# Performance work log

Hardware: AMD Instinct MI355X
Metric: run time of the kernel (lower is better)

The kernel has to match this reference:

```python
import jax, jax.numpy as jnp
from jax import lax
import numpy as np


def _sobel(x):
    """|sobel_x(x)| + |sobel_y(x)| with zero padding. x: [N,C,H,W].
    Implemented as ONE depthwise conv (replaces the per-batch/per-channel
    conv2d loops in the torch Sobelxy module; math is identical)."""
    N, C, H, W = x.shape
    kx = jnp.array([[-1., 0., 1.], [-2., 0., 2.], [-1., 0., 1.]], x.dtype)
    ky = jnp.array([[1., 2., 1.], [0., 0., 0.], [-1., -2., -1.]], x.dtype)
    k = jnp.tile(jnp.stack([kx, ky]), (C, 1, 1))[:, None]  # [2C,1,3,3]
    o = lax.conv_general_dilated(x, k, (1, 1), ((1, 1), (1, 1)),
                                 feature_group_count=C)  # [N,2C,H,W]
    o = o.reshape(N, C, 2, H, W)
    return jnp.abs(o[:, :, 0]) + jnp.abs(o[:, :, 1])


def setup_inputs() -> dict:
    B, C, H, W, NL = 4, 1, 640, 640, 10
    key = jax.random.key(0)
    k1, k2, k3, k4 = jax.random.split(key, 4)
    image_vis = jax.random.uniform(k1, (B, C, H, W), jnp.float32)
    image_ir = jax.random.uniform(k2, (B, 1, H, W), jnp.float32)
    generate_img = jax.random.uniform(k3, (B, C, H, W), jnp.float32)
    LW_th = jax.random.uniform(k4, (B, 1, H, W), jnp.float32)
    # labels: (cls, x1, y1, x2, y2); all-zero coords => ignored box
    rng = np.random.default_rng(0)
    lab = np.zeros((B, NL, 5), np.int32)
    for bi in range(B):
        n = int(rng.integers(3, NL + 1))
        x1 = rng.integers(0, W // 2, n)
        y1 = rng.integers(0, H // 2, n)
        x2 = np.minimum(x1 + rng.integers(16, W // 2, n), W)
        y2 = np.minimum(y1 + rng.integers(16, H // 2, n), H)
        lab[bi, :n, 1] = x1; lab[bi, :n, 2] = y1
        lab[bi, :n, 3] = x2; lab[bi, :n, 4] = y2
    return {"b": jnp.float32(0.5), "c": jnp.float32(0.5),
            "image_vis": image_vis, "image_ir": image_ir,
            "generate_img": generate_img, "label": jnp.asarray(lab),
            "LW_th": LW_th}


def reference(b, c, image_vis, image_ir, generate_img, label, LW_th):
    alpha, beta = b, c
    B, C, H, W = image_vis.shape
    NL = label.shape[1]
    image_y = image_vis
    image_th = jnp.broadcast_to(LW_th, (B, C, H, W))

    x_in_mean = 0.5 * image_y + 0.5 * image_th
    x_in_mean_7 = 0.3 * image_y + 0.7 * image_th
    x_in_mean_max = jnp.maximum(image_y, x_in_mean)

    y_grad = _sobel(image_y)
    x_in_mean_grad = _sobel(x_in_mean)
    gen_grad = _sobel(generate_img)
    x_grad_joint = jnp.maximum(y_grad, x_in_mean_grad)

    # global per-sample L1 losses (F.l1_loss per batch element = mean over CHW)
    loss_in = jnp.mean(jnp.abs(generate_img - x_in_mean_max), axis=(1, 2, 3))
    loss_grad = jnp.mean(jnp.abs(gen_grad - x_grad_joint), axis=(1, 2, 3))
    loss_global = alpha * loss_in + (1 - alpha) * loss_grad

    # ---- per-box losses via masking (exactly equals crop + zero-padded Sobel:
    # Sobel(crop) inside the box == Sobel(mask*image) inside the box) ----
    x1 = label[..., 1]; y1 = label[..., 2]  # [B,NL]
    x2 = label[..., 3]; y2 = label[..., 4]
    valid = ~((x1 == 0) & (y1 == 0) & (x2 == 0) & (y2 == 0))
    rows = jnp.arange(H); cols = jnp.arange(W)
    rmask = (rows[None, None, :] >= y1[..., None]) & (rows[None, None, :] < y2[..., None])
    cmask = (cols[None, None, :] >= x1[..., None]) & (cols[None, None, :] < x2[..., None])
    mask = (rmask[..., :, None] & cmask[..., None, :]).astype(image_y.dtype)  # [B,NL,H,W]
    mask5 = mask[:, :, None]  # [B,NL,1,H,W]

    def boxed(img):  # [B,C,H,W] -> masked [B*NL,C,H,W]
        return (img[:, None] * mask5).reshape(B * NL, C, H, W)

    m_vis = boxed(image_y)
    m_mean = boxed(x_in_mean_7)
    m_gen = boxed(generate_img)
    g_vis = _sobel(m_vis)
    g_mean = _sobel(m_mean)
    g_gen = _sobel(m_gen)
    g_max = jnp.maximum(g_vis, g_mean)
    in_max = jnp.maximum(m_vis, m_mean)

    fmask = mask.reshape(B * NL, 1, H, W)
    area = ((y2 - y1) * (x2 - x1)).reshape(B * NL).astype(image_y.dtype) * C
    safe_area = jnp.maximum(area, 1.0)
    Lssim = jnp.sum(jnp.abs(g_gen - g_max) * fmask, axis=(1, 2, 3)) / safe_area
    L1loss = jnp.sum(jnp.abs(m_gen - in_max) * fmask, axis=(1, 2, 3)) / safe_area
    v = valid.reshape(B * NL).astype(image_y.dtype)
    Lssim = (Lssim * v).reshape(B, NL)
    L1loss = (L1loss * v).reshape(B, NL)

    exist = ((Lssim != 0) | (L1loss != 0)).astype(image_y.dtype)
    cnt = exist.sum(axis=1)
    safe_cnt = jnp.maximum(cnt, 1.0)
    ls = jnp.where(cnt > 0, Lssim.sum(axis=1) / safe_cnt, 0.0)
    lin = jnp.where(cnt > 0, L1loss.sum(axis=1) / safe_cnt, 0.0)
    loss_label = (1 - beta) * ls + beta * lin

    loss_ss = jnp.zeros((B,), image_y.dtype)
    return (loss_ss, loss_global, loss_label, loss_in, loss_grad, ls, lin)
```

## Files before the change

### kernel.cpp

```cpp
#include <hip/hip_runtime.h>

#define BB    4
#define HH    640
#define WW    640
#define NLB   10
#define HWSZ  (HH * WW)
#define BLK   128
#define PR    8
#define GT    5
#define GBANDS (HH / PR)
#define GPB   (GT * GBANDS)
#define GBLK  (GPB * BB)
#define BOXSLOTS 40
#define XBLK  (BB * NLB * BOXSLOTS)

__device__ __forceinline__ void reduce2_write(float vin, float vgr,
                                              float* __restrict__ dst) {
    #pragma unroll
    for (int off = 32; off > 0; off >>= 1) {
        vin += __shfl_down(vin, off);
        vgr += __shfl_down(vgr, off);
    }
    __shared__ float s0[2], s1[2];
    const int lane = threadIdx.x & 63;
    const int w    = threadIdx.x >> 6;
    if (lane == 0) { s0[w] = vin; s1[w] = vgr; }
    __syncthreads();
    if (threadIdx.x == 0) {
        dst[0] = s0[0] + s0[1];
        dst[1] = s1[0] + s1[1];
    }
}

#define SOB(P, S) \
    (fabsf((P[S][2] - P[S][0]) + 2.0f * (P[S+1][2] - P[S+1][0]) + (P[S+2][2] - P[S+2][0])) + \
     fabsf((P[S][0] + 2.0f * P[S][1] + P[S][2]) - (P[S+2][0] + 2.0f * P[S+2][1] + P[S+2][2])))

__global__ __launch_bounds__(BLK) void kmain(const float* __restrict__ vis,
                                             const float* __restrict__ th,
                                             const float* __restrict__ gen,
                                             const int* __restrict__ label,
                                             float* __restrict__ gpart,
                                             float* __restrict__ xpart) {
    const int t = threadIdx.x;
    if (blockIdx.x < GBLK) {
        const int gid  = blockIdx.x;
        const int b    = gid / GPB;
        const int rem  = gid % GPB;
        const int band = rem / GT;
        const int xt   = rem % GT;
        const int c    = xt * BLK + t;
        const int r0   = band * PR;
        const float* v = vis + b * HWSZ;
        const float* tp = th + b * HWSZ;
        const float* g = gen + b * HWSZ;
        const bool okL = (c >= 1);
        const bool okR = (c + 1 < WW);

        float rv[PR + 2][3], rt[PR + 2][3], rg[PR + 2][3];
        #pragma unroll
        for (int i = 0; i < PR + 2; ++i) {
            const int rr = r0 - 1 + i;
            const bool rok = ((unsigned)rr < (unsigned)HH);
            const int base = rr * WW + c;
            rv[i][0] = (rok && okL) ? v[base - 1]  : 0.0f;
            rv[i][1] =  rok         ? v[base]      : 0.0f;
            rv[i][2] = (rok && okR) ? v[base + 1]  : 0.0f;
            rt[i][0] = (rok && okL) ? tp[base - 1] : 0.0f;
            rt[i][1] =  rok         ? tp[base]     : 0.0f;
            rt[i][2] = (rok && okR) ? tp[base + 1] : 0.0f;
            rg[i][0] = (rok && okL) ? g[base - 1]  : 0.0f;
            rg[i][1] =  rok         ? g[base]      : 0.0f;
            rg[i][2] = (rok && okR) ? g[base + 1]  : 0.0f;
        }
        float t_in = 0.0f, t_gr = 0.0f;
        #pragma unroll
        for (int s = 0; s < PR; ++s) {
            float m[3][3];
            #pragma unroll
            for (int i = 0; i < 3; ++i)
                #pragma unroll
                for (int j = 0; j < 3; ++j)
                    m[i][j] = 0.5f * rv[s + i][j] + 0.5f * rt[s + i][j];
            const float sv = SOB(rv, s);
            const float sg = SOB(rg, s);
            const float sm = SOB(m, 0);
            t_gr += fabsf(sg - fmaxf(sv, sm));
            t_in += fabsf(rg[s + 1][1] - fmaxf(rv[s + 1][1], m[1][1]));
        }
        reduce2_write(t_in, t_gr, gpart + gid * 2);
    } else {
        const int q    = blockIdx.x - GBLK;
        const int box  = q / BOXSLOTS;
        const int slot = q % BOXSLOTS;
        const int b    = box / NLB;
        const int* lb  = label + box * 5;
        const int x1 = lb[1], y1 = lb[2], x2 = lb[3], y2 = lb[4];
        const float* v = vis + b * HWSZ;
        const float* tp = th + b * HWSZ;
        const float* g = gen + b * HWSZ;
        float t_in = 0.0f, t_gr = 0.0f;
        for (int r0 = y1 + slot * PR; r0 < y2; r0 += BOXSLOTS * PR) {
            for (int cb = x1; cb < x2; cb += BLK) {
                const int c = cb + t;
                const bool okL = (c > x1) && (c - 1 < x2);
                const bool okC = (c < x2);
                const bool okR = (c + 1 < x2);
                float rv[PR + 2][3], rt[PR + 2][3], rg[PR + 2][3];
                #pragma unroll
                for (int i = 0; i < PR + 2; ++i) {
                    const int rr = r0 - 1 + i;
                    const bool rok = (rr >= y1) && (rr < y2);
                    const int base = rr * WW + c;
                    rv[i][0] = (rok && okL) ? v[base - 1]  : 0.0f;
                    rv[i][1] = (rok && okC) ? v[base]      : 0.0f;
                    rv[i][2] = (rok && okR) ? v[base + 1]  : 0.0f;
                    rt[i][0] = (rok && okL) ? tp[base - 1] : 0.0f;
                    rt[i][1] = (rok && okC) ? tp[base]     : 0.0f;
                    rt[i][2] = (rok && okR) ? tp[base + 1] : 0.0f;
                    rg[i][0] = (rok && okL) ? g[base - 1]  : 0.0f;
                    rg[i][1] = (rok && okC) ? g[base]      : 0.0f;
                    rg[i][2] = (rok && okR) ? g[base + 1]  : 0.0f;
                }
                #pragma unroll
                for (int s = 0; s < PR; ++s) {
                    const float inb = (okC && (r0 + s < y2)) ? 1.0f : 0.0f;
                    float m[3][3];
                    #pragma unroll
                    for (int i = 0; i < 3; ++i)
                        #pragma unroll
                        for (int j = 0; j < 3; ++j)
                            m[i][j] = 0.3f * rv[s + i][j] + 0.7f * rt[s + i][j];
                    const float sv = SOB(rv, s);
                    const float sg = SOB(rg, s);
                    const float sm = SOB(m, 0);
                    t_gr += inb * fabsf(sg - fmaxf(sv, sm));
                    t_in += inb * fabsf(rg[s + 1][1] - fmaxf(rv[s + 1][1], m[1][1]));
                }
            }
        }
        reduce2_write(t_in, t_gr, xpart + q * 2);
    }
}

__global__ __launch_bounds__(256) void kfin(const float* __restrict__ gpart,
                                            const float* __restrict__ xpart,
                                            const int* __restrict__ label,
                                            const float* __restrict__ bptr,
                                            const float* __restrict__ cptr,
                                            float* __restrict__ out) {
    const int t = threadIdx.x;
    __shared__ float Sin[BB], Sgr[BB];
    __shared__ float Ls[BB * NLB], L1[BB * NLB];
    {
        const int w = t >> 6, l = t & 63;
        float a = 0.0f, gr = 0.0f;
        for (int j = l; j < GPB; j += 64) {
            a  += gpart[(w * GPB + j) * 2 + 0];
            gr += gpart[(w * GPB + j) * 2 + 1];
        }
        #pragma unroll
        for (int off = 32; off > 0; off >>= 1) {
            a  += __shfl_down(a, off);
            gr += __shfl_down(gr, off);
        }
        if (l == 0) { Sin[w] = a; Sgr[w] = gr; }
    }
    if (t < BB * NLB) {
        float si = 0.0f, sg = 0.0f;
        for (int s = 0; s < BOXSLOTS; ++s) {
            si += xpart[(t * BOXSLOTS + s) * 2 + 0];
            sg += xpart[(t * BOXSLOTS + s) * 2 + 1];
        }
        const int* lb = label + t * 5;
        const int x1 = lb[1], y1 = lb[2], x2 = lb[3], y2 = lb[4];
        const bool valid = !((x1 == 0) && (y1 == 0) && (x2 == 0) && (y2 == 0));
        const float area = (float)((y2 - y1) * (x2 - x1));
        const float safe_area = fmaxf(area, 1.0f);
        const float vv = valid ? 1.0f : 0.0f;
        Ls[t] = sg / safe_area * vv;
        L1[t] = si / safe_area * vv;
    }
    __syncthreads();
    if (t < BB) {
        const float alpha = bptr[0];
        const float beta  = cptr[0];
        float cnt = 0.0f, sls = 0.0f, slin = 0.0f;
        for (int nl = 0; nl < NLB; nl++) {
            const float a = Ls[t * NLB + nl];
            const float l = L1[t * NLB + nl];
            if (a != 0.0f || l != 0.0f) cnt += 1.0f;
            sls  += a;
            slin += l;
        }
        const float safe_cnt = fmaxf(cnt, 1.0f);
        const float ls  = (cnt > 0.0f) ? (sls  / safe_cnt) : 0.0f;
        const float lin = (cnt > 0.0f) ? (slin / safe_cnt) : 0.0f;
        const float loss_label = (1.0f - beta) * ls + beta * lin;
        const float loss_in    = Sin[t] * (1.0f / (float)HWSZ);
        const float loss_grad  = Sgr[t] * (1.0f / (float)HWSZ);
        const float loss_global = alpha * loss_in + (1.0f - alpha) * loss_grad;
        out[0      + t] = 0.0f;
        out[BB     + t] = loss_global;
        out[2 * BB + t] = loss_label;
        out[3 * BB + t] = loss_in;
        out[4 * BB + t] = loss_grad;
        out[5 * BB + t] = ls;
        out[6 * BB + t] = lin;
    }
}

extern "C" void kernel_launch(void* const* d_in, const int* in_sizes, int n_in,
                              void* d_out, int out_size, void* d_ws, size_t ws_size,
                              hipStream_t stream) {
    const float* bptr  = (const float*)d_in[0];
    const float* cptr  = (const float*)d_in[1];
    const float* vis   = (const float*)d_in[2];
    const float* gen   = (const float*)d_in[4];
    const int*   label = (const int*)d_in[5];
    const float* th    = (const float*)d_in[6];
    float* out = (float*)d_out;

    float* gpart = (float*)d_ws;
    float* xpart = gpart + GBLK * 2;

    kmain<<<GBLK + XBLK, BLK, 0, stream>>>(vis, th, gen, label, gpart, xpart);
    kfin<<<1, 256, 0, stream>>>(gpart, xpart, label, bptr, cptr, out);
}
```

Measured before the change: 117.5 us.

## Compute 4x4 pixel strips per thread with float4 loads and linear Sobel of the blend

Each thread now covers a 4-column by 4-row strip instead of one column by 8 rows. It loads each input row with one aligned float4 plus two scalar edge values, which cuts the redundant overlapping neighbour loads of the old one-column layout. The blended image's Sobel gradients are built as weighted sums of the vis and th gradients, so the blended 3x3 window is no longer formed separately. The global-sum path launches half as many blocks, and the box path aligns its start column to 4. In exchange each thread holds more registers, and many threads in box blocks sit idle because a block now spans 512 columns.

```diff
diff --git a/kernel.cpp b/kernel.cpp
--- a/kernel.cpp
+++ b/kernel.cpp
@@ -1,18 +1,19 @@
 #include <hip/hip_runtime.h>
 
-#define BB    4
-#define HH    640
-#define WW    640
-#define NLB   10
-#define HWSZ  (HH * WW)
-#define BLK   128
-#define PR    8
-#define GT    5
-#define GBANDS (HH / PR)
-#define GPB   (GT * GBANDS)
-#define GBLK  (GPB * BB)
-#define BOXSLOTS 40
-#define XBLK  (BB * NLB * BOXSLOTS)
+#define BB     4
+#define HH     640
+#define WW     640
+#define NLB    10
+#define HWSZ   (HH * WW)
+#define BLK    128
+#define PRX    4
+#define GXT    160
+#define GBANDS 160
+#define GSIDS  (BB * GBANDS * GXT)
+#define GBLKS  (GSIDS / BLK)
+#define GPBB   (GBLKS / BB)
+#define SLOTS  40
+#define XBLKS  (BB * NLB * SLOTS)
 
 __device__ __forceinline__ void reduce2_write(float vin, float vgr,
                                               float* __restrict__ dst) {
@@ -32,9 +33,71 @@
     }
 }
 
-#define SOB(P, S) \
-    (fabsf((P[S][2] - P[S][0]) + 2.0f * (P[S+1][2] - P[S+1][0]) + (P[S+2][2] - P[S+2][0])) + \
-     fabsf((P[S][0] + 2.0f * P[S][1] + P[S][2]) - (P[S+2][0] + 2.0f * P[S+2][1] + P[S+2][2])))
+__device__ __forceinline__ void strip4(const float* __restrict__ v,
+                                       const float* __restrict__ t,
+                                       const float* __restrict__ g,
+                                       int c0, int r0, int ry1, int ry2,
+                                       int cx1, int cx2, float w0, float w1,
+                                       float& s_in, float& s_gr) {
+    float A[3][PRX + 2][6];
+    const int c4 = min(max(c0, 0), WW - 4);
+    const int cl = max(c0 - 1, 0);
+    const int cr = min(c0 + 4, WW - 1);
+    bool okc[6];
+    #pragma unroll
+    for (int j = 0; j < 6; ++j) {
+        const int cc = c0 - 1 + j;
+        okc[j] = (cc >= cx1) && (cc < cx2);
+    }
+    const float* P[3] = { v, t, g };
+    #pragma unroll
+    for (int i = 0; i < PRX + 2; ++i) {
+        const int rr  = r0 - 1 + i;
+        const bool rok = (rr >= ry1) && (rr < ry2);
+        const int rb  = min(max(rr, 0), HH - 1) * WW;
+        #pragma unroll
+        for (int p = 0; p < 3; ++p) {
+            const float4 f = *(const float4*)(P[p] + rb + c4);
+            const float eL = P[p][rb + cl];
+            const float eR = P[p][rb + cr];
+            A[p][i][0] = (rok && okc[0]) ? eL  : 0.0f;
+            A[p][i][1] = (rok && okc[1]) ? f.x : 0.0f;
+            A[p][i][2] = (rok && okc[2]) ? f.y : 0.0f;
+            A[p][i][3] = (rok && okc[3]) ? f.z : 0.0f;
+            A[p][i][4] = (rok && okc[4]) ? f.w : 0.0f;
+            A[p][i][5] = (rok && okc[5]) ? eR  : 0.0f;
+        }
+    }
+    #pragma unroll
+    for (int s = 0; s < PRX; ++s) {
+        const int rc = r0 + s;
+        const bool rcin = (rc >= ry1) && (rc < ry2);
+        #pragma unroll
+        for (int c = 0; c < 4; ++c) {
+            float gx[3], gy[3];
+            #pragma unroll
+            for (int p = 0; p < 3; ++p) {
+                gx[p] = (A[p][s][c + 2] - A[p][s][c])
+                      + 2.0f * (A[p][s + 1][c + 2] - A[p][s + 1][c])
+                      + (A[p][s + 2][c + 2] - A[p][s + 2][c]);
+                gy[p] = (A[p][s][c] + 2.0f * A[p][s][c + 1] + A[p][s][c + 2])
+                      - (A[p][s + 2][c] + 2.0f * A[p][s + 2][c + 1] + A[p][s + 2][c + 2]);
+            }
+            const float sv  = fabsf(gx[0]) + fabsf(gy[0]);
+            const float sg  = fabsf(gx[2]) + fabsf(gy[2]);
+            const float gxm = w0 * gx[0] + w1 * gx[1];
+            const float gym = w0 * gy[0] + w1 * gy[1];
+            const float sm  = fabsf(gxm) + fabsf(gym);
+            const float vc  = A[0][s + 1][c + 1];
+            const float tc  = A[1][s + 1][c + 1];
+            const float gc  = A[2][s + 1][c + 1];
+            const float mc  = w0 * vc + w1 * tc;
+            const float inb = (rcin && okc[c + 1]) ? 1.0f : 0.0f;
+            s_gr += inb * fabsf(sg - fmaxf(sv, sm));
+            s_in += inb * fabsf(gc - fmaxf(vc, mc));
+        }
+    }
+}
 
 __global__ __launch_bounds__(BLK) void kmain(const float* __restrict__ vis,
                                              const float* __restrict__ th,
@@ -43,103 +106,31 @@
                                              float* __restrict__ gpart,
                                              float* __restrict__ xpart) {
     const int t = threadIdx.x;
-    if (blockIdx.x < GBLK) {
-        const int gid  = blockIdx.x;
-        const int b    = gid / GPB;
-        const int rem  = gid % GPB;
-        const int band = rem / GT;
-        const int xt   = rem % GT;
-        const int c    = xt * BLK + t;
-        const int r0   = band * PR;
-        const float* v = vis + b * HWSZ;
-        const float* tp = th + b * HWSZ;
-        const float* g = gen + b * HWSZ;
-        const bool okL = (c >= 1);
-        const bool okR = (c + 1 < WW);
-
-        float rv[PR + 2][3], rt[PR + 2][3], rg[PR + 2][3];
-        #pragma unroll
-        for (int i = 0; i < PR + 2; ++i) {
-            const int rr = r0 - 1 + i;
-            const bool rok = ((unsigned)rr < (unsigned)HH);
-            const int base = rr * WW + c;
-            rv[i][0] = (rok && okL) ? v[base - 1]  : 0.0f;
-            rv[i][1] =  rok         ? v[base]      : 0.0f;
-            rv[i][2] = (rok && okR) ? v[base + 1]  : 0.0f;
-            rt[i][0] = (rok && okL) ? tp[base - 1] : 0.0f;
-            rt[i][1] =  rok         ? tp[base]     : 0.0f;
-            rt[i][2] = (rok && okR) ? tp[base + 1] : 0.0f;
-            rg[i][0] = (rok && okL) ? g[base - 1]  : 0.0f;
-            rg[i][1] =  rok         ? g[base]      : 0.0f;
-            rg[i][2] = (rok && okR) ? g[base + 1]  : 0.0f;
-        }
-        float t_in = 0.0f, t_gr = 0.0f;
-        #pragma unroll
-        for (int s = 0; s < PR; ++s) {
-            float m[3][3];
-            #pragma unroll
-            for (int i = 0; i < 3; ++i)
-                #pragma unroll
-                for (int j = 0; j < 3; ++j)
-                    m[i][j] = 0.5f * rv[s + i][j] + 0.5f * rt[s + i][j];
-            const float sv = SOB(rv, s);
-            const float sg = SOB(rg, s);
-            const float sm = SOB(m, 0);
-            t_gr += fabsf(sg - fmaxf(sv, sm));
-            t_in += fabsf(rg[s + 1][1] - fmaxf(rv[s + 1][1], m[1][1]));
-        }
-        reduce2_write(t_in, t_gr, gpart + gid * 2);
+    float s_in = 0.0f, s_gr = 0.0f;
+    if (blockIdx.x < GBLKS) {
+        const int sid  = blockIdx.x * BLK + t;
+        const int xt   = sid % GXT;
+        const int band = (sid / GXT) % GBANDS;
+        const int b    = sid / (GXT * GBANDS);
+        strip4(vis + b * HWSZ, th + b * HWSZ, gen + b * HWSZ,
+               4 * xt, 4 * band, 0, HH, 0, WW, 0.5f, 0.5f, s_in, s_gr);
+        reduce2_write(s_in, s_gr, gpart + blockIdx.x * 2);
     } else {
-        const int q    = blockIdx.x - GBLK;
-        const int box  = q / BOXSLOTS;
-        const int slot = q % BOXSLOTS;
+        const int q    = blockIdx.x - GBLKS;
+        const int box  = q / SLOTS;
+        const int slot = q % SLOTS;
         const int b    = box / NLB;
         const int* lb  = label + box * 5;
         const int x1 = lb[1], y1 = lb[2], x2 = lb[3], y2 = lb[4];
-        const float* v = vis + b * HWSZ;
-        const float* tp = th + b * HWSZ;
-        const float* g = gen + b * HWSZ;
-        float t_in = 0.0f, t_gr = 0.0f;
-        for (int r0 = y1 + slot * PR; r0 < y2; r0 += BOXSLOTS * PR) {
-            for (int cb = x1; cb < x2; cb += BLK) {
-                const int c = cb + t;
-                const bool okL = (c > x1) && (c - 1 < x2);
-                const bool okC = (c < x2);
-                const bool okR = (c + 1 < x2);
-                float rv[PR + 2][3], rt[PR + 2][3], rg[PR + 2][3];
-                #pragma unroll
-                for (int i = 0; i < PR + 2; ++i) {
-                    const int rr = r0 - 1 + i;
-                    const bool rok = (rr >= y1) && (rr < y2);
-                    const int base = rr * WW + c;
-                    rv[i][0] = (rok && okL) ? v[base - 1]  : 0.0f;
-                    rv[i][1] = (rok && okC) ? v[base]      : 0.0f;
-                    rv[i][2] = (rok && okR) ? v[base + 1]  : 0.0f;
-                    rt[i][0] = (rok && okL) ? tp[base - 1] : 0.0f;
-                    rt[i][1] = (rok && okC) ? tp[base]     : 0.0f;
-                    rt[i][2] = (rok && okR) ? tp[base + 1] : 0.0f;
-                    rg[i][0] = (rok && okL) ? g[base - 1]  : 0.0f;
-                    rg[i][1] = (rok && okC) ? g[base]      : 0.0f;
-                    rg[i][2] = (rok && okR) ? g[base + 1]  : 0.0f;
-                }
-                #pragma unroll
-                for (int s = 0; s < PR; ++s) {
-                    const float inb = (okC && (r0 + s < y2)) ? 1.0f : 0.0f;
-                    float m[3][3];
-                    #pragma unroll
-                    for (int i = 0; i < 3; ++i)
-                        #pragma unroll
-                        for (int j = 0; j < 3; ++j)
-                            m[i][j] = 0.3f * rv[s + i][j] + 0.7f * rt[s + i][j];
-                    const float sv = SOB(rv, s);
-                    const float sg = SOB(rg, s);
-                    const float sm = SOB(m, 0);
-                    t_gr += inb * fabsf(sg - fmaxf(sv, sm));
-                    t_in += inb * fabsf(rg[s + 1][1] - fmaxf(rv[s + 1][1], m[1][1]));
-                }
-            }
-        }
-        reduce2_write(t_in, t_gr, xpart + q * 2);
+        const int x1a = x1 & ~3;
+        const float* v  = vis + b * HWSZ;
+        const float* tp = th  + b * HWSZ;
+        const float* g  = gen + b * HWSZ;
+        for (int r0 = y1 + slot * PRX; r0 < y2; r0 += SLOTS * PRX)
+            for (int cb = x1a; cb < x2; cb += BLK * 4)
+                strip4(v, tp, g, cb + 4 * t, r0, y1, y2, x1, x2,
+                       0.3f, 0.7f, s_in, s_gr);
+        reduce2_write(s_in, s_gr, xpart + q * 2);
     }
 }
 
@@ -155,9 +146,9 @@
     {
         const int w = t >> 6, l = t & 63;
         float a = 0.0f, gr = 0.0f;
-        for (int j = l; j < GPB; j += 64) {
-            a  += gpart[(w * GPB + j) * 2 + 0];
-            gr += gpart[(w * GPB + j) * 2 + 1];
+        for (int j = l; j < GPBB; j += 64) {
+            a  += gpart[(w * GPBB + j) * 2 + 0];
+            gr += gpart[(w * GPBB + j) * 2 + 1];
         }
         #pragma unroll
         for (int off = 32; off > 0; off >>= 1) {
@@ -168,9 +159,9 @@
     }
     if (t < BB * NLB) {
         float si = 0.0f, sg = 0.0f;
-        for (int s = 0; s < BOXSLOTS; ++s) {
-            si += xpart[(t * BOXSLOTS + s) * 2 + 0];
-            sg += xpart[(t * BOXSLOTS + s) * 2 + 1];
+        for (int s = 0; s < SLOTS; ++s) {
+            si += xpart[(t * SLOTS + s) * 2 + 0];
+            sg += xpart[(t * SLOTS + s) * 2 + 1];
         }
         const int* lb = label + t * 5;
         const int x1 = lb[1], y1 = lb[2], x2 = lb[3], y2 = lb[4];
@@ -222,8 +213,8 @@
     float* out = (float*)d_out;
 
     float* gpart = (float*)d_ws;
-    float* xpart = gpart + GBLK * 2;
-
-    kmain<<<GBLK + XBLK, BLK, 0, stream>>>(vis, th, gen, label, gpart, xpart);
+    float* xpart = gpart + GBLKS * 2;
+
+    kmain<<<GBLKS + XBLKS, BLK, 0, stream>>>(vis, th, gen, label, gpart, xpart);
     kfin<<<1, 256, 0, stream>>>(gpart, xpart, label, bptr, cptr, out);
 }
```

Result: faster. 105.1 us (-10.6%).
